# Kernel tuning notes

Measured on AMD Instinct MI355X. Metric: run time of the kernel, lower is better.

Reference implementation:

```python
import jax, jax.numpy as jnp
import numpy as np

HQ = 32      # query heads
HKV = 8      # kv heads
DH = 128     # head dim
B, S, D = 8, 1, 4096
MAX_SEQ = 4096


def rope(x, pos):
    """Rotary embedding on interleaved pairs. x: [B,S,H,dh], pos: [S] int."""
    d = x.shape[-1]
    theta = 1.0 / (10000.0 ** (jnp.arange(0, d, 2, dtype=jnp.float32) / d))  # [d/2]
    ang = pos[:, None].astype(jnp.float32) * theta[None, :]                  # [S,d/2]
    cos = jnp.cos(ang)[None, :, None, :]
    sin = jnp.sin(ang)[None, :, None, :]
    xr, xi = x[..., 0::2], x[..., 1::2]
    out_r = xr * cos - xi * sin
    out_i = xr * sin + xi * cos
    return jnp.stack([out_r, out_i], axis=-1).reshape(x.shape)


def setup_inputs() -> dict:
    key = jax.random.key(0)
    ks = jax.random.split(key, 8)
    s = 0.02
    return {
        "x": jax.random.normal(ks[0], (B, S, D), jnp.float32),
        "wq": jax.random.normal(ks[1], (D, HQ * DH), jnp.float32) * s,
        "bq": jnp.zeros((HQ * DH,), jnp.float32),
        "wk": jax.random.normal(ks[2], (D, HKV * DH), jnp.float32) * s,
        "bk": jnp.zeros((HKV * DH,), jnp.float32),
        "wv": jax.random.normal(ks[3], (D, HKV * DH), jnp.float32) * s,
        "bv": jnp.zeros((HKV * DH,), jnp.float32),
        "wo": jax.random.normal(ks[4], (HQ * DH, D), jnp.float32) * s,
        "bo": jnp.zeros((D,), jnp.float32),
        "cache_k": jax.random.normal(ks[5], (B, MAX_SEQ, HKV, DH), jnp.float32) * 0.5,
        "cache_v": jax.random.normal(ks[6], (B, MAX_SEQ, HKV, DH), jnp.float32) * 0.5,
        "start_pos": MAX_SEQ - S,  # decode step at end of cache
    }


def reference(x, wq, bq, wk, bk, wv, bv, wo, bo, cache_k, cache_v, start_pos):
    b, s, d = x.shape
    n_rep = HQ // HKV
    q = (x @ wq + bq).reshape(b, s, HQ, DH)
    k = (x @ wk + bk).reshape(b, s, HKV, DH)
    v = (x @ wv + bv).reshape(b, s, HKV, DH)
    pos = start_pos + jnp.arange(s)
    q = rope(q, pos)
    k = rope(k, pos)
    # KV-cache scatter write
    cache_k = jax.lax.dynamic_update_slice(cache_k, k, (0, start_pos, 0, 0))
    cache_v = jax.lax.dynamic_update_slice(cache_v, v, (0, start_pos, 0, 0))
    t = start_pos + s  # static (start_pos is a Python int)
    keys = cache_k[:, :t]    # [B,T,HKV,DH]
    values = cache_v[:, :t]
    # repeat_kv: duplicate each kv head n_rep times -> [B,T,HQ,DH]
    keys = jnp.repeat(keys, n_rep, axis=2)
    values = jnp.repeat(values, n_rep, axis=2)
    # naive softmax attention, score matrix materialized
    scores = jnp.einsum("bshd,bthd->bhst", q, keys) * (DH ** -0.5)  # [B,HQ,S,T]
    attn = jax.nn.softmax(scores, axis=-1)
    out = jnp.einsum("bhst,bthd->bshd", attn, values).reshape(b, s, HQ * DH)
    return out @ wo + bo
```

## Files before the change

### kernel.cpp

```cpp
#include <hip/hip_runtime.h>
#include <cmath>

#define NB 8
#define DIM 4096
#define NHQ 32
#define NHKV 8
#define NDH 128
#define MAXSEQ 4096
#define STARTPOS 4095
#define QKV_COLS 6144
#define RCHUNK 64
#define NRC 64
#define SCALE 0.08838834764831845f

__global__ __launch_bounds__(256) void qkv_partial_k(
    const float* __restrict__ x, const float* __restrict__ wq,
    const float* __restrict__ wk, const float* __restrict__ wv,
    float* __restrict__ part) {
  int bid = blockIdx.x;
  int ct = bid % 12, rc = bid / 12;
  int tid = threadIdx.x;
  const float* W; int ldw; int colbase;
  int gcolbase = ct * 512;
  if (ct < 8)       { W = wq; ldw = NHQ * NDH;  colbase = gcolbase; }
  else if (ct < 10) { W = wk; ldw = NHKV * NDH; colbase = gcolbase - 4096; }
  else              { W = wv; ldw = NHKV * NDH; colbase = gcolbase - 5120; }

  __shared__ __align__(16) float xs[RCHUNK][8];
  int rbase = rc * RCHUNK;
  for (int i = tid; i < RCHUNK * 8; i += 256) {
    int b = i >> 6, r = i & 63;
    xs[r][b] = x[b * DIM + rbase + r];
  }
  __syncthreads();

  int col = colbase + tid * 2;
  const float* wp = W + (size_t)rbase * ldw + col;
  float2 acc[8];
#pragma unroll
  for (int b = 0; b < 8; b++) { acc[b].x = 0.f; acc[b].y = 0.f; }

#pragma unroll 8
  for (int r = 0; r < RCHUNK; r++) {
    float2 w2 = *(const float2*)wp; wp += ldw;
    float4 xa = *(const float4*)&xs[r][0];
    float4 xb = *(const float4*)&xs[r][4];
    acc[0].x += xa.x * w2.x; acc[0].y += xa.x * w2.y;
    acc[1].x += xa.y * w2.x; acc[1].y += xa.y * w2.y;
    acc[2].x += xa.z * w2.x; acc[2].y += xa.z * w2.y;
    acc[3].x += xa.w * w2.x; acc[3].y += xa.w * w2.y;
    acc[4].x += xb.x * w2.x; acc[4].y += xb.x * w2.y;
    acc[5].x += xb.y * w2.x; acc[5].y += xb.y * w2.y;
    acc[6].x += xb.z * w2.x; acc[6].y += xb.z * w2.y;
    acc[7].x += xb.w * w2.x; acc[7].y += xb.w * w2.y;
  }
  int gcol = gcolbase + tid * 2;
#pragma unroll
  for (int b = 0; b < 8; b++)
    *(float2*)&part[((size_t)rc * 8 + b) * QKV_COLS + gcol] = acc[b];
}

__global__ __launch_bounds__(256) void qkv_reduce_rope_k(
    const float* __restrict__ part, const float* __restrict__ bq,
    const float* __restrict__ bk, const float* __restrict__ bv,
    float* __restrict__ qws, float* __restrict__ kws, float* __restrict__ vws) {
  int idx = blockIdx.x * 256 + threadIdx.x;
  int b = idx / QKV_COLS, col = idx % QKV_COLS;
  float s = 0.f;
#pragma unroll 8
  for (int rcc = 0; rcc < NRC; rcc++)
    s += part[((size_t)rcc * 8 + b) * QKV_COLS + col];
  float bias = (col < 4096) ? bq[col] : (col < 5120 ? bk[col - 4096] : bv[col - 5120]);
  s += bias;
  float outv = s;
  if (col < 5120) {
    int dim = col & 127;
    int i2 = dim & ~1;
    float theta = powf(10000.f, -(float)i2 * (1.f / 128.f));
    float ang = (float)STARTPOS * theta;
    float c = cosf(ang), sn = sinf(ang);
    float other = __shfl_xor(s, 1);
    if ((col & 1) == 0) outv = s * c - other * sn;
    else                outv = other * sn + s * c;
  }
  if (col < 4096)       qws[b * 4096 + col] = outv;
  else if (col < 5120)  kws[b * 1024 + (col - 4096)] = outv;
  else                  vws[b * 1024 + (col - 5120)] = outv;
}

__global__ __launch_bounds__(256) void attn_partial_k(
    const float* __restrict__ q, const float* __restrict__ kws,
    const float* __restrict__ vws, const float* __restrict__ ck,
    const float* __restrict__ cv, float* __restrict__ pm,
    float* __restrict__ pl, float* __restrict__ pacc) {
  int bid = blockIdx.x;
  int chunk = bid & 15, grp = bid >> 4;
  int b = grp >> 3, hkv = grp & 7;
  int tid = threadIdx.x;
  int wv_ = tid >> 6, lane = tid & 63;

  __shared__ float sbuf[4][256];

  int tchunk = chunk * 256;

  {
    int t = tchunk + tid;
    const float* kr = (t == STARTPOS)
        ? (kws + ((size_t)b * NHKV + hkv) * NDH)
        : (ck + (((size_t)b * MAXSEQ + t) * NHKV + hkv) * NDH);
    const float* qg = q + ((size_t)b * NHQ + hkv * 4) * NDH;
    float a0 = 0.f, a1 = 0.f, a2 = 0.f, a3 = 0.f;
#pragma unroll 8
    for (int j = 0; j < 32; j++) {
      float4 kv = *(const float4*)(kr + 4 * j);
      float4 q0 = *(const float4*)(qg + 4 * j);
      float4 q1 = *(const float4*)(qg + 128 + 4 * j);
      float4 q2 = *(const float4*)(qg + 256 + 4 * j);
      float4 q3 = *(const float4*)(qg + 384 + 4 * j);
      a0 += kv.x * q0.x + kv.y * q0.y + kv.z * q0.z + kv.w * q0.w;
      a1 += kv.x * q1.x + kv.y * q1.y + kv.z * q1.z + kv.w * q1.w;
      a2 += kv.x * q2.x + kv.y * q2.y + kv.z * q2.z + kv.w * q2.w;
      a3 += kv.x * q3.x + kv.y * q3.y + kv.z * q3.z + kv.w * q3.w;
    }
    sbuf[0][tid] = a0 * SCALE;
    sbuf[1][tid] = a1 * SCALE;
    sbuf[2][tid] = a2 * SCALE;
    sbuf[3][tid] = a3 * SCALE;
  }
  __syncthreads();

  float e0 = sbuf[wv_][lane];
  float e1 = sbuf[wv_][lane + 64];
  float e2 = sbuf[wv_][lane + 128];
  float e3 = sbuf[wv_][lane + 192];
  float m = fmaxf(fmaxf(e0, e1), fmaxf(e2, e3));
#pragma unroll
  for (int off = 32; off; off >>= 1) m = fmaxf(m, __shfl_xor(m, off));
  float p0 = expf(e0 - m), p1 = expf(e1 - m), p2 = expf(e2 - m), p3 = expf(e3 - m);
  float l = p0 + p1 + p2 + p3;
#pragma unroll
  for (int off = 32; off; off >>= 1) l += __shfl_xor(l, off);
  sbuf[wv_][lane] = p0;
  sbuf[wv_][lane + 64] = p1;
  sbuf[wv_][lane + 128] = p2;
  sbuf[wv_][lane + 192] = p3;
  if (lane == 0) {
    pm[((size_t)grp * 16 + chunk) * 4 + wv_] = m;
    pl[((size_t)grp * 16 + chunk) * 4 + wv_] = l;
  }

  int half = lane >> 5;
  int dq = (lane & 31) * 4;
  float4 acc = {0.f, 0.f, 0.f, 0.f};
  const float* vb = cv + (((size_t)b * MAXSEQ + tchunk) * NHKV + hkv) * NDH;
  for (int tt = 0; tt < 256; tt += 16) {
#pragma unroll
    for (int u = 0; u < 8; u++) {
      int tl = tt + u * 2 + half;
      int tg = tchunk + tl;
      const float* vr = (tg == STARTPOS)
          ? (vws + ((size_t)b * NHKV + hkv) * NDH)
          : (vb + (size_t)tl * (NHKV * NDH));
      float4 v4 = *(const float4*)(vr + dq);
      float p = sbuf[wv_][tl];
      acc.x += p * v4.x;
      acc.y += p * v4.y;
      acc.z += p * v4.z;
      acc.w += p * v4.w;
    }
  }
  acc.x += __shfl_xor(acc.x, 32);
  acc.y += __shfl_xor(acc.y, 32);
  acc.z += __shfl_xor(acc.z, 32);
  acc.w += __shfl_xor(acc.w, 32);
  if (half == 0)
    *(float4*)&pacc[(((size_t)grp * 16 + chunk) * 4 + wv_) * NDH + dq] = acc;
}

__global__ __launch_bounds__(128) void attn_combine_k(
    const float* __restrict__ pm, const float* __restrict__ pl,
    const float* __restrict__ pacc, float* __restrict__ aout) {
  int bid = blockIdx.x;
  int b = bid >> 5, hq = bid & 31;
  int grp = b * 8 + (hq >> 2), r = hq & 3;
  int d = threadIdx.x;
  float mv[16];
  float M = -1e30f;
#pragma unroll
  for (int c = 0; c < 16; c++) {
    mv[c] = pm[((size_t)grp * 16 + c) * 4 + r];
    M = fmaxf(M, mv[c]);
  }
  float L = 0.f;
  float w[16];
#pragma unroll
  for (int c = 0; c < 16; c++) {
    w[c] = expf(mv[c] - M);
    L += w[c] * pl[((size_t)grp * 16 + c) * 4 + r];
  }
  float o = 0.f;
#pragma unroll
  for (int c = 0; c < 16; c++)
    o += w[c] * pacc[(((size_t)grp * 16 + c) * 4 + r) * NDH + d];
  aout[(size_t)b * 4096 + hq * NDH + d] = o / L;
}

__global__ __launch_bounds__(256) void out_partial_k(
    const float* __restrict__ ain, const float* __restrict__ wo,
    float* __restrict__ part) {
  int bid = blockIdx.x;
  int ct = bid & 7, rc = bid >> 3;
  int tid = threadIdx.x;
  __shared__ __align__(16) float xs[RCHUNK][8];
  int rbase = rc * RCHUNK;
  for (int i = tid; i < RCHUNK * 8; i += 256) {
    int b = i >> 6, r = i & 63;
    xs[r][b] = ain[(size_t)b * 4096 + rbase + r];
  }
  __syncthreads();

  int col = ct * 512 + tid * 2;
  const float* wp = wo + (size_t)rbase * 4096 + col;
  float2 acc[8];
#pragma unroll
  for (int b = 0; b < 8; b++) { acc[b].x = 0.f; acc[b].y = 0.f; }
#pragma unroll 8
  for (int r = 0; r < RCHUNK; r++) {
    float2 w2 = *(const float2*)wp; wp += 4096;
    float4 xa = *(const float4*)&xs[r][0];
    float4 xb = *(const float4*)&xs[r][4];
    acc[0].x += xa.x * w2.x; acc[0].y += xa.x * w2.y;
    acc[1].x += xa.y * w2.x; acc[1].y += xa.y * w2.y;
    acc[2].x += xa.z * w2.x; acc[2].y += xa.z * w2.y;
    acc[3].x += xa.w * w2.x; acc[3].y += xa.w * w2.y;
    acc[4].x += xb.x * w2.x; acc[4].y += xb.x * w2.y;
    acc[5].x += xb.y * w2.x; acc[5].y += xb.y * w2.y;
    acc[6].x += xb.z * w2.x; acc[6].y += xb.z * w2.y;
    acc[7].x += xb.w * w2.x; acc[7].y += xb.w * w2.y;
  }
#pragma unroll
  for (int b = 0; b < 8; b++)
    *(float2*)&part[((size_t)rc * 8 + b) * 4096 + col] = acc[b];
}

__global__ __launch_bounds__(256) void out_reduce_k(
    const float* __restrict__ part, const float* __restrict__ bo,
    float* __restrict__ out) {
  int idx = blockIdx.x * 256 + threadIdx.x;
  int b = idx >> 12, col = idx & 4095;
  float s = bo[col];
#pragma unroll 8
  for (int rcc = 0; rcc < NRC; rcc++)
    s += part[((size_t)rcc * 8 + b) * 4096 + col];
  out[idx] = s;
  (void)b;
}

extern "C" void kernel_launch(void* const* d_in, const int* in_sizes, int n_in,
                              void* d_out, int out_size, void* d_ws, size_t ws_size,
                              hipStream_t stream) {
  const float* x       = (const float*)d_in[0];
  const float* wq      = (const float*)d_in[1];
  const float* bq      = (const float*)d_in[2];
  const float* wk      = (const float*)d_in[3];
  const float* bk      = (const float*)d_in[4];
  const float* wv      = (const float*)d_in[5];
  const float* bv      = (const float*)d_in[6];
  const float* wo      = (const float*)d_in[7];
  const float* bo      = (const float*)d_in[8];
  const float* cache_k = (const float*)d_in[9];
  const float* cache_v = (const float*)d_in[10];
  float* out = (float*)d_out;

  float* ws = (float*)d_ws;
  float* qkv_part = ws;
  float* wo_part  = ws;
  float* qws  = ws + 3145728;
  float* kws  = qws + 32768;
  float* vws  = kws + 8192;
  float* pm   = vws + 8192;
  float* pl   = pm + 4096;
  float* pacc = pl + 4096;
  float* aout = pacc + 524288;

  qkv_partial_k<<<768, 256, 0, stream>>>(x, wq, wk, wv, qkv_part);
  qkv_reduce_rope_k<<<192, 256, 0, stream>>>(qkv_part, bq, bk, bv, qws, kws, vws);
  attn_partial_k<<<1024, 256, 0, stream>>>(qws, kws, vws, cache_k, cache_v, pm, pl, pacc);
  attn_combine_k<<<256, 128, 0, stream>>>(pm, pl, pacc, aout);
  out_partial_k<<<512, 256, 0, stream>>>(aout, wo, wo_part);
  out_reduce_k<<<128, 256, 0, stream>>>(wo_part, bo, out);
}
```

Baseline: 112.9 us.

## Split attention into smaller chunks, stage q in LDS, and hoist new-token V fixup

Halves the attention chunk to 128 positions, doubling the block count to 2048 and the partial-combine fan-in to 32. Q is staged in shared memory, and each thread computes two heads' scores for one position instead of four heads. The per-iteration STARTPOS branch in the V loop is replaced by a single correction term applied only in the last chunk, which removes a select from the hot loop. The aim is more parallelism and memory-level concurrency for the bandwidth-bound KV read. The cost is extra combine work, a larger workspace, and each K row now being loaded by two threads.

```diff
diff --git a/kernel.cpp b/kernel.cpp
--- a/kernel.cpp
+++ b/kernel.cpp
@@ -12,6 +12,10 @@
 #define RCHUNK 64
 #define NRC 64
 #define SCALE 0.08838834764831845f
+#define NCHUNK 32
+#define CPOS 128
+
+#define DOT4(k, qq) ((k).x*(qq).x + (k).y*(qq).y + (k).z*(qq).z + (k).w*(qq).w)
 
 __global__ __launch_bounds__(256) void qkv_partial_k(
     const float* __restrict__ x, const float* __restrict__ wq,
@@ -88,93 +92,107 @@
   else                  vws[b * 1024 + (col - 5120)] = outv;
 }
 
-__global__ __launch_bounds__(256) void attn_partial_k(
+__global__ __launch_bounds__(256, 4) void attn_partial_k(
     const float* __restrict__ q, const float* __restrict__ kws,
     const float* __restrict__ vws, const float* __restrict__ ck,
     const float* __restrict__ cv, float* __restrict__ pm,
     float* __restrict__ pl, float* __restrict__ pacc) {
   int bid = blockIdx.x;
-  int chunk = bid & 15, grp = bid >> 4;
+  int chunk = bid & 31, grp = bid >> 5;
   int b = grp >> 3, hkv = grp & 7;
   int tid = threadIdx.x;
   int wv_ = tid >> 6, lane = tid & 63;
 
-  __shared__ float sbuf[4][256];
-
-  int tchunk = chunk * 256;
+  __shared__ float sbuf[4][CPOS];
+  __shared__ __align__(16) float qs[4][NDH];
+
+  for (int i = tid; i < 512; i += 256) {
+    int h = i >> 7, d = i & 127;
+    qs[h][d] = q[((size_t)b * NHQ + hkv * 4 + h) * NDH + d];
+  }
+  __syncthreads();
+
+  int tchunk = chunk * CPOS;
 
   {
-    int t = tchunk + tid;
+    int pos = tid & 127;
+    int hp = tid >> 7;
+    int h0 = hp * 2;
+    int t = tchunk + pos;
     const float* kr = (t == STARTPOS)
         ? (kws + ((size_t)b * NHKV + hkv) * NDH)
         : (ck + (((size_t)b * MAXSEQ + t) * NHKV + hkv) * NDH);
-    const float* qg = q + ((size_t)b * NHQ + hkv * 4) * NDH;
-    float a0 = 0.f, a1 = 0.f, a2 = 0.f, a3 = 0.f;
-#pragma unroll 8
-    for (int j = 0; j < 32; j++) {
-      float4 kv = *(const float4*)(kr + 4 * j);
-      float4 q0 = *(const float4*)(qg + 4 * j);
-      float4 q1 = *(const float4*)(qg + 128 + 4 * j);
-      float4 q2 = *(const float4*)(qg + 256 + 4 * j);
-      float4 q3 = *(const float4*)(qg + 384 + 4 * j);
-      a0 += kv.x * q0.x + kv.y * q0.y + kv.z * q0.z + kv.w * q0.w;
-      a1 += kv.x * q1.x + kv.y * q1.y + kv.z * q1.z + kv.w * q1.w;
-      a2 += kv.x * q2.x + kv.y * q2.y + kv.z * q2.z + kv.w * q2.w;
-      a3 += kv.x * q3.x + kv.y * q3.y + kv.z * q3.z + kv.w * q3.w;
+    const float4* kr4 = (const float4*)kr;
+    const float4* qa4 = (const float4*)&qs[h0][0];
+    const float4* qb4 = (const float4*)&qs[h0 + 1][0];
+    float a0 = 0.f, a1 = 0.f;
+#pragma unroll
+    for (int j4 = 0; j4 < 32; j4 += 4) {
+      float4 k0 = kr4[j4 + 0];
+      float4 k1 = kr4[j4 + 1];
+      float4 k2 = kr4[j4 + 2];
+      float4 k3 = kr4[j4 + 3];
+      float4 qa0 = qa4[j4 + 0], qa1 = qa4[j4 + 1], qa2 = qa4[j4 + 2], qa3 = qa4[j4 + 3];
+      float4 qb0 = qb4[j4 + 0], qb1 = qb4[j4 + 1], qb2 = qb4[j4 + 2], qb3 = qb4[j4 + 3];
+      a0 += DOT4(k0, qa0) + DOT4(k1, qa1) + DOT4(k2, qa2) + DOT4(k3, qa3);
+      a1 += DOT4(k0, qb0) + DOT4(k1, qb1) + DOT4(k2, qb2) + DOT4(k3, qb3);
     }
-    sbuf[0][tid] = a0 * SCALE;
-    sbuf[1][tid] = a1 * SCALE;
-    sbuf[2][tid] = a2 * SCALE;
-    sbuf[3][tid] = a3 * SCALE;
+    __syncthreads();
+    sbuf[h0][pos] = a0 * SCALE;
+    sbuf[h0 + 1][pos] = a1 * SCALE;
   }
   __syncthreads();
 
   float e0 = sbuf[wv_][lane];
   float e1 = sbuf[wv_][lane + 64];
-  float e2 = sbuf[wv_][lane + 128];
-  float e3 = sbuf[wv_][lane + 192];
-  float m = fmaxf(fmaxf(e0, e1), fmaxf(e2, e3));
+  float m = fmaxf(e0, e1);
 #pragma unroll
   for (int off = 32; off; off >>= 1) m = fmaxf(m, __shfl_xor(m, off));
-  float p0 = expf(e0 - m), p1 = expf(e1 - m), p2 = expf(e2 - m), p3 = expf(e3 - m);
-  float l = p0 + p1 + p2 + p3;
+  float p0 = expf(e0 - m), p1 = expf(e1 - m);
+  float l = p0 + p1;
 #pragma unroll
   for (int off = 32; off; off >>= 1) l += __shfl_xor(l, off);
   sbuf[wv_][lane] = p0;
   sbuf[wv_][lane + 64] = p1;
-  sbuf[wv_][lane + 128] = p2;
-  sbuf[wv_][lane + 192] = p3;
   if (lane == 0) {
-    pm[((size_t)grp * 16 + chunk) * 4 + wv_] = m;
-    pl[((size_t)grp * 16 + chunk) * 4 + wv_] = l;
+    pm[((size_t)grp * NCHUNK + chunk) * 4 + wv_] = m;
+    pl[((size_t)grp * NCHUNK + chunk) * 4 + wv_] = l;
   }
 
   int half = lane >> 5;
   int dq = (lane & 31) * 4;
   float4 acc = {0.f, 0.f, 0.f, 0.f};
   const float* vb = cv + (((size_t)b * MAXSEQ + tchunk) * NHKV + hkv) * NDH;
-  for (int tt = 0; tt < 256; tt += 16) {
-#pragma unroll
-    for (int u = 0; u < 8; u++) {
-      int tl = tt + u * 2 + half;
-      int tg = tchunk + tl;
-      const float* vr = (tg == STARTPOS)
-          ? (vws + ((size_t)b * NHKV + hkv) * NDH)
-          : (vb + (size_t)tl * (NHKV * NDH));
-      float4 v4 = *(const float4*)(vr + dq);
-      float p = sbuf[wv_][tl];
-      acc.x += p * v4.x;
-      acc.y += p * v4.y;
-      acc.z += p * v4.z;
-      acc.w += p * v4.w;
-    }
+#pragma unroll 4
+  for (int tt = 0; tt < CPOS; tt += 8) {
+    float4 v0 = *(const float4*)(vb + (size_t)(tt + 0 + half) * 1024 + dq);
+    float4 v1 = *(const float4*)(vb + (size_t)(tt + 2 + half) * 1024 + dq);
+    float4 v2 = *(const float4*)(vb + (size_t)(tt + 4 + half) * 1024 + dq);
+    float4 v3 = *(const float4*)(vb + (size_t)(tt + 6 + half) * 1024 + dq);
+    float pp0 = sbuf[wv_][tt + 0 + half];
+    float pp1 = sbuf[wv_][tt + 2 + half];
+    float pp2 = sbuf[wv_][tt + 4 + half];
+    float pp3 = sbuf[wv_][tt + 6 + half];
+    acc.x += pp0 * v0.x + pp1 * v1.x + pp2 * v2.x + pp3 * v3.x;
+    acc.y += pp0 * v0.y + pp1 * v1.y + pp2 * v2.y + pp3 * v3.y;
+    acc.z += pp0 * v0.z + pp1 * v1.z + pp2 * v2.z + pp3 * v3.z;
+    acc.w += pp0 * v0.w + pp1 * v1.w + pp2 * v2.w + pp3 * v3.w;
+  }
+  if (chunk == 31 && half == 1) {
+    float pp = sbuf[wv_][127];
+    float4 vold = *(const float4*)(vb + (size_t)127 * 1024 + dq);
+    float4 vnew = *(const float4*)(vws + ((size_t)b * NHKV + hkv) * NDH + dq);
+    acc.x += pp * (vnew.x - vold.x);
+    acc.y += pp * (vnew.y - vold.y);
+    acc.z += pp * (vnew.z - vold.z);
+    acc.w += pp * (vnew.w - vold.w);
   }
   acc.x += __shfl_xor(acc.x, 32);
   acc.y += __shfl_xor(acc.y, 32);
   acc.z += __shfl_xor(acc.z, 32);
   acc.w += __shfl_xor(acc.w, 32);
   if (half == 0)
-    *(float4*)&pacc[(((size_t)grp * 16 + chunk) * 4 + wv_) * NDH + dq] = acc;
+    *(float4*)&pacc[(((size_t)grp * NCHUNK + chunk) * 4 + wv_) * NDH + dq] = acc;
 }
 
 __global__ __launch_bounds__(128) void attn_combine_k(
@@ -184,24 +202,24 @@
   int b = bid >> 5, hq = bid & 31;
   int grp = b * 8 + (hq >> 2), r = hq & 3;
   int d = threadIdx.x;
-  float mv[16];
+  float mv[NCHUNK];
   float M = -1e30f;
 #pragma unroll
-  for (int c = 0; c < 16; c++) {
-    mv[c] = pm[((size_t)grp * 16 + c) * 4 + r];
+  for (int c = 0; c < NCHUNK; c++) {
+    mv[c] = pm[((size_t)grp * NCHUNK + c) * 4 + r];
     M = fmaxf(M, mv[c]);
   }
   float L = 0.f;
-  float w[16];
-#pragma unroll
-  for (int c = 0; c < 16; c++) {
+  float w[NCHUNK];
+#pragma unroll
+  for (int c = 0; c < NCHUNK; c++) {
     w[c] = expf(mv[c] - M);
-    L += w[c] * pl[((size_t)grp * 16 + c) * 4 + r];
+    L += w[c] * pl[((size_t)grp * NCHUNK + c) * 4 + r];
   }
   float o = 0.f;
 #pragma unroll
-  for (int c = 0; c < 16; c++)
-    o += w[c] * pacc[(((size_t)grp * 16 + c) * 4 + r) * NDH + d];
+  for (int c = 0; c < NCHUNK; c++)
+    o += w[c] * pacc[(((size_t)grp * NCHUNK + c) * 4 + r) * NDH + d];
   aout[(size_t)b * 4096 + hq * NDH + d] = o / L;
 }
 
@@ -279,13 +297,13 @@
   float* kws  = qws + 32768;
   float* vws  = kws + 8192;
   float* pm   = vws + 8192;
-  float* pl   = pm + 4096;
-  float* pacc = pl + 4096;
-  float* aout = pacc + 524288;
+  float* pl   = pm + 8192;
+  float* pacc = pl + 8192;
+  float* aout = pacc + 1048576;
 
   qkv_partial_k<<<768, 256, 0, stream>>>(x, wq, wk, wv, qkv_part);
   qkv_reduce_rope_k<<<192, 256, 0, stream>>>(qkv_part, bq, bk, bv, qws, kws, vws);
-  attn_partial_k<<<1024, 256, 0, stream>>>(qws, kws, vws, cache_k, cache_v, pm, pl, pacc);
+  attn_partial_k<<<2048, 256, 0, stream>>>(qws, kws, vws, cache_k, cache_v, pm, pl, pacc);
   attn_combine_k<<<256, 128, 0, stream>>>(pm, pl, pacc, aout);
   out_partial_k<<<512, 256, 0, stream>>>(aout, wo, wo_part);
   out_reduce_k<<<128, 256, 0, stream>>>(wo_part, bo, out);
```

New measurement: 137.1 us. 21.4% more time.

## Rewrite decode attention as flash-style kernel with async double-buffered LDS staging

Applied to the files above, without the earlier changes.

Replaces the two-pass chunked attention kernel with a flash-style kernel that walks 1024 timesteps per block in 64-row tiles. It keeps a running max and sum for an online softmax. K and V tiles are staged into double-buffered LDS with global_load_lds, using an XOR swizzle on K to avoid bank conflicts. Fewer chunks per head group (4 instead of 16) shrink the partial results the combine kernel has to merge. The cost is roughly 128KB of LDS per block, which allows only one block per CU, plus a sync and a rescale on every tile, so latency hiding depends on the async copies.

```diff
diff --git a/kernel.cpp b/kernel.cpp
--- a/kernel.cpp
+++ b/kernel.cpp
@@ -12,6 +12,14 @@
 #define RCHUNK 64
 #define NRC 64
 #define SCALE 0.08838834764831845f
+
+#define DOT4(k, qq) ((k).x*(qq).x + (k).y*(qq).y + (k).z*(qq).z + (k).w*(qq).w)
+
+__device__ __forceinline__ void gl_lds16(const float* g, float* l) {
+  __builtin_amdgcn_global_load_lds(
+      (const __attribute__((address_space(1))) unsigned int*)g,
+      (__attribute__((address_space(3))) unsigned int*)l, 16, 0, 0);
+}
 
 __global__ __launch_bounds__(256) void qkv_partial_k(
     const float* __restrict__ x, const float* __restrict__ wq,
@@ -88,93 +96,100 @@
   else                  vws[b * 1024 + (col - 5120)] = outv;
 }
 
-__global__ __launch_bounds__(256) void attn_partial_k(
-    const float* __restrict__ q, const float* __restrict__ kws,
+__global__ __launch_bounds__(256) void flash_k(
+    const float* __restrict__ qws, const float* __restrict__ kws,
     const float* __restrict__ vws, const float* __restrict__ ck,
     const float* __restrict__ cv, float* __restrict__ pm,
     float* __restrict__ pl, float* __restrict__ pacc) {
   int bid = blockIdx.x;
-  int chunk = bid & 15, grp = bid >> 4;
-  int b = grp >> 3, hkv = grp & 7;
+  int group = bid >> 2, chunk = bid & 3;
+  int b = group >> 3, hkv = group & 7;
   int tid = threadIdx.x;
-  int wv_ = tid >> 6, lane = tid & 63;
-
-  __shared__ float sbuf[4][256];
-
-  int tchunk = chunk * 256;
-
-  {
-    int t = tchunk + tid;
-    const float* kr = (t == STARTPOS)
-        ? (kws + ((size_t)b * NHKV + hkv) * NDH)
-        : (ck + (((size_t)b * MAXSEQ + t) * NHKV + hkv) * NDH);
-    const float* qg = q + ((size_t)b * NHQ + hkv * 4) * NDH;
-    float a0 = 0.f, a1 = 0.f, a2 = 0.f, a3 = 0.f;
-#pragma unroll 8
+  int w = tid >> 6, lane = tid & 63;
+
+  __shared__ __align__(16) float kbuf[2][64][128];
+  __shared__ __align__(16) float vbuf[2][64][128];
+  __shared__ __align__(16) float qs[4][128];
+  __shared__ float pbuf[4][64];
+
+  if (tid < 128) {
+    int h = tid >> 5, d4 = (tid & 31) * 4;
+    *(float4*)&qs[h][d4] =
+        *(const float4*)(qws + ((size_t)b * NHQ + hkv * 4 + h) * NDH + d4);
+  }
+
+  const int t0c = chunk * 1024;
+  const int srow8 = tid >> 5;
+  const int slot  = tid & 31;
+  const float* kwsrow = kws + ((size_t)b * NHKV + hkv) * NDH;
+  const float* vwsrow = vws + ((size_t)b * NHKV + hkv) * NDH;
+
+#define STAGE(bufi_, tile_) do {                                              \
+    int tb_ = t0c + (tile_) * 64;                                             \
+    float* kdst_ = &kbuf[bufi_][0][0] + w * 256;                              \
+    float* vdst_ = &vbuf[bufi_][0][0] + w * 256;                              \
+    _Pragma("unroll")                                                         \
+    for (int i_ = 0; i_ < 8; i_++) {                                          \
+      int row_ = i_ * 8 + srow8;                                              \
+      int t_ = tb_ + row_;                                                    \
+      int ks_ = slot ^ (row_ & 7);                                            \
+      const float* kg_ = (t_ == STARTPOS) ? (kwsrow + ks_ * 4)                \
+          : (ck + ((size_t)(b * MAXSEQ + t_) * NHKV + hkv) * NDH + ks_ * 4);  \
+      gl_lds16(kg_, kdst_ + i_ * 1024);                                       \
+      const float* vg_ = (t_ == STARTPOS) ? (vwsrow + slot * 4)               \
+          : (cv + ((size_t)(b * MAXSEQ + t_) * NHKV + hkv) * NDH + slot * 4); \
+      gl_lds16(vg_, vdst_ + i_ * 1024);                                       \
+    }                                                                         \
+  } while (0)
+
+  float2 acc = {0.f, 0.f};
+  float m_run = -1e30f, l_run = 0.f;
+
+  STAGE(0, 0);
+
+  for (int tile = 0; tile < 16; ++tile) {
+    int bufi = tile & 1;
+    __syncthreads();
+    if (tile < 15) STAGE(bufi ^ 1, tile + 1);
+
+    float s = 0.f;
+#pragma unroll
     for (int j = 0; j < 32; j++) {
-      float4 kv = *(const float4*)(kr + 4 * j);
-      float4 q0 = *(const float4*)(qg + 4 * j);
-      float4 q1 = *(const float4*)(qg + 128 + 4 * j);
-      float4 q2 = *(const float4*)(qg + 256 + 4 * j);
-      float4 q3 = *(const float4*)(qg + 384 + 4 * j);
-      a0 += kv.x * q0.x + kv.y * q0.y + kv.z * q0.z + kv.w * q0.w;
-      a1 += kv.x * q1.x + kv.y * q1.y + kv.z * q1.z + kv.w * q1.w;
-      a2 += kv.x * q2.x + kv.y * q2.y + kv.z * q2.z + kv.w * q2.w;
-      a3 += kv.x * q3.x + kv.y * q3.y + kv.z * q3.z + kv.w * q3.w;
+      float4 kf = *(const float4*)&kbuf[bufi][lane][4 * (j ^ (lane & 7))];
+      float4 qf = *(const float4*)&qs[w][j * 4];
+      s += DOT4(kf, qf);
     }
-    sbuf[0][tid] = a0 * SCALE;
-    sbuf[1][tid] = a1 * SCALE;
-    sbuf[2][tid] = a2 * SCALE;
-    sbuf[3][tid] = a3 * SCALE;
-  }
-  __syncthreads();
-
-  float e0 = sbuf[wv_][lane];
-  float e1 = sbuf[wv_][lane + 64];
-  float e2 = sbuf[wv_][lane + 128];
-  float e3 = sbuf[wv_][lane + 192];
-  float m = fmaxf(fmaxf(e0, e1), fmaxf(e2, e3));
-#pragma unroll
-  for (int off = 32; off; off >>= 1) m = fmaxf(m, __shfl_xor(m, off));
-  float p0 = expf(e0 - m), p1 = expf(e1 - m), p2 = expf(e2 - m), p3 = expf(e3 - m);
-  float l = p0 + p1 + p2 + p3;
-#pragma unroll
-  for (int off = 32; off; off >>= 1) l += __shfl_xor(l, off);
-  sbuf[wv_][lane] = p0;
-  sbuf[wv_][lane + 64] = p1;
-  sbuf[wv_][lane + 128] = p2;
-  sbuf[wv_][lane + 192] = p3;
+    s *= SCALE;
+
+    float mt = s;
+#pragma unroll
+    for (int off = 32; off; off >>= 1) mt = fmaxf(mt, __shfl_xor(mt, off));
+    float mn = fmaxf(m_run, mt);
+    float al = expf(m_run - mn);
+    float p = expf(s - mn);
+    float lt = p;
+#pragma unroll
+    for (int off = 32; off; off >>= 1) lt += __shfl_xor(lt, off);
+    l_run = l_run * al + lt;
+    m_run = mn;
+    pbuf[w][lane] = p;
+    acc.x *= al; acc.y *= al;
+
+#pragma unroll 8
+    for (int t = 0; t < 64; t++) {
+      float pp = pbuf[w][t];
+      float2 v2 = *(const float2*)&vbuf[bufi][t][lane * 2];
+      acc.x += pp * v2.x;
+      acc.y += pp * v2.y;
+    }
+  }
+#undef STAGE
+
+  *(float2*)&pacc[((size_t)bid * 4 + w) * NDH + lane * 2] = acc;
   if (lane == 0) {
-    pm[((size_t)grp * 16 + chunk) * 4 + wv_] = m;
-    pl[((size_t)grp * 16 + chunk) * 4 + wv_] = l;
-  }
-
-  int half = lane >> 5;
-  int dq = (lane & 31) * 4;
-  float4 acc = {0.f, 0.f, 0.f, 0.f};
-  const float* vb = cv + (((size_t)b * MAXSEQ + tchunk) * NHKV + hkv) * NDH;
-  for (int tt = 0; tt < 256; tt += 16) {
-#pragma unroll
-    for (int u = 0; u < 8; u++) {
-      int tl = tt + u * 2 + half;
-      int tg = tchunk + tl;
-      const float* vr = (tg == STARTPOS)
-          ? (vws + ((size_t)b * NHKV + hkv) * NDH)
-          : (vb + (size_t)tl * (NHKV * NDH));
-      float4 v4 = *(const float4*)(vr + dq);
-      float p = sbuf[wv_][tl];
-      acc.x += p * v4.x;
-      acc.y += p * v4.y;
-      acc.z += p * v4.z;
-      acc.w += p * v4.w;
-    }
-  }
-  acc.x += __shfl_xor(acc.x, 32);
-  acc.y += __shfl_xor(acc.y, 32);
-  acc.z += __shfl_xor(acc.z, 32);
-  acc.w += __shfl_xor(acc.w, 32);
-  if (half == 0)
-    *(float4*)&pacc[(((size_t)grp * 16 + chunk) * 4 + wv_) * NDH + dq] = acc;
+    pm[bid * 4 + w] = m_run;
+    pl[bid * 4 + w] = l_run;
+  }
 }
 
 __global__ __launch_bounds__(128) void attn_combine_k(
@@ -182,26 +197,26 @@
     const float* __restrict__ pacc, float* __restrict__ aout) {
   int bid = blockIdx.x;
   int b = bid >> 5, hq = bid & 31;
-  int grp = b * 8 + (hq >> 2), r = hq & 3;
+  int group = b * 8 + (hq >> 2), r = hq & 3;
   int d = threadIdx.x;
-  float mv[16];
+  float mv[4];
   float M = -1e30f;
 #pragma unroll
-  for (int c = 0; c < 16; c++) {
-    mv[c] = pm[((size_t)grp * 16 + c) * 4 + r];
+  for (int c = 0; c < 4; c++) {
+    mv[c] = pm[(group * 4 + c) * 4 + r];
     M = fmaxf(M, mv[c]);
   }
   float L = 0.f;
-  float w[16];
-#pragma unroll
-  for (int c = 0; c < 16; c++) {
-    w[c] = expf(mv[c] - M);
-    L += w[c] * pl[((size_t)grp * 16 + c) * 4 + r];
+  float wgt[4];
+#pragma unroll
+  for (int c = 0; c < 4; c++) {
+    wgt[c] = expf(mv[c] - M);
+    L += wgt[c] * pl[(group * 4 + c) * 4 + r];
   }
   float o = 0.f;
 #pragma unroll
-  for (int c = 0; c < 16; c++)
-    o += w[c] * pacc[(((size_t)grp * 16 + c) * 4 + r) * NDH + d];
+  for (int c = 0; c < 4; c++)
+    o += wgt[c] * pacc[((size_t)(group * 4 + c) * 4 + r) * NDH + d];
   aout[(size_t)b * 4096 + hq * NDH + d] = o / L;
 }
 
@@ -276,16 +291,16 @@
   float* qkv_part = ws;
   float* wo_part  = ws;
   float* qws  = ws + 3145728;
-  float* kws  = qws + 32768;
-  float* vws  = kws + 8192;
-  float* pm   = vws + 8192;
-  float* pl   = pm + 4096;
-  float* pacc = pl + 4096;
-  float* aout = pacc + 524288;
+  float* kws  = ws + 3178496;
+  float* vws  = ws + 3186688;
+  float* pm   = ws + 3194880;
+  float* pl   = ws + 3195904;
+  float* pacc = ws + 3196928;
+  float* aout = ws + 3328000;
 
   qkv_partial_k<<<768, 256, 0, stream>>>(x, wq, wk, wv, qkv_part);
   qkv_reduce_rope_k<<<192, 256, 0, stream>>>(qkv_part, bq, bk, bv, qws, kws, vws);
-  attn_partial_k<<<1024, 256, 0, stream>>>(qws, kws, vws, cache_k, cache_v, pm, pl, pacc);
+  flash_k<<<256, 256, 0, stream>>>(qws, kws, vws, cache_k, cache_v, pm, pl, pacc);
   attn_combine_k<<<256, 128, 0, stream>>>(pm, pl, pacc, aout);
   out_partial_k<<<512, 256, 0, stream>>>(aout, wo, wo_part);
   out_reduce_k<<<128, 256, 0, stream>>>(wo_part, bo, out);
```

After: 141.3 us. 1.25x slower.
